# Performance work log

Hardware: AMD Instinct MI355X
Metric: run time of the kernel (lower is better)

The kernel has to match this reference:

```python
import jax, jax.numpy as jnp
import numpy as np

EPS = 1e-5

def _bn(x, gamma, beta, mean, var):
    # channel axis = 1; inference-style batchnorm with given stats
    shape = (1, -1) + (1,) * (x.ndim - 2)
    inv = gamma / jnp.sqrt(var + EPS)
    return x * inv.reshape(shape) + (beta - mean * inv).reshape(shape)

def _gather(f, idx):
    # f: (C, N), idx: (N, ns) -> (C, N, ns)
    return f[:, idx]

def setup_inputs() -> dict:
    key = jax.random.key(0)
    ks = jax.random.split(key, 24)
    B, N, C, NS, O = 4, 32768, 64, 16, 128
    inp = {}
    inp['xyz'] = jax.random.normal(ks[0], (B, N, 3), jnp.float32)
    inp['feature'] = jax.random.normal(ks[1], (B, C, N), jnp.float32)
    inp['idx'] = jax.random.randint(ks[2], (B, N, NS), 0, N, jnp.int64 if jax.config.jax_enable_x64 else jnp.int32)
    inp['W1'] = jax.random.normal(ks[3], (64, 3), jnp.float32)
    inp['b1'] = jax.random.normal(ks[4], (64,), jnp.float32)
    inp['g1'] = jax.random.uniform(ks[5], (64,), jnp.float32)
    inp['be1'] = jax.random.normal(ks[6], (64,), jnp.float32)
    inp['m1'] = jnp.zeros((64,), jnp.float32)
    inp['v1'] = jnp.ones((64,), jnp.float32)
    inp['W2'] = jax.random.normal(ks[7], (64, 64), jnp.float32)
    inp['b2'] = jax.random.normal(ks[8], (64,), jnp.float32)
    inp['g2'] = jax.random.uniform(ks[9], (64,), jnp.float32)
    inp['be2'] = jax.random.normal(ks[10], (64,), jnp.float32)
    inp['m2'] = jnp.zeros((64,), jnp.float32)
    inp['v2'] = jnp.ones((64,), jnp.float32)
    inp['W3'] = jax.random.normal(ks[11], (64, 64), jnp.float32)
    inp['b3'] = jax.random.normal(ks[12], (64,), jnp.float32)
    inp['Wf'] = jax.random.normal(ks[13], (O, C * 64), jnp.float32)
    inp['bf'] = jax.random.normal(ks[14], (O,), jnp.float32)
    inp['gf'] = jax.random.uniform(ks[15], (O,), jnp.float32)
    inp['bef'] = jax.random.normal(ks[16], (O,), jnp.float32)
    inp['mf'] = jnp.zeros((O,), jnp.float32)
    inp['vf'] = jnp.ones((O,), jnp.float32)
    return inp

def reference(xyz, feature, idx, W1, b1, g1, be1, m1, v1, W2, b2, g2, be2, m2, v2, W3, b3, Wf, bf, gf, bef, mf, vf):
    B, C, N = feature.shape
    xyz_t = jnp.transpose(xyz, (0, 2, 1))  # (B, 3, N)
    # grouped relative positions: (B, 3, N, ns)
    grouped_xyz = jax.vmap(_gather)(xyz_t, idx) - xyz_t[:, :, :, None]
    # WeightNet: Conv2d 1x1 layers on channel dim
    h = jnp.einsum('oc,bcns->bons', W1, grouped_xyz) + b1[None, :, None, None]
    h = jax.nn.relu(_bn(h, g1, be1, m1, v1))
    h = jnp.einsum('oc,bcns->bons', W2, h) + b2[None, :, None, None]
    h = jax.nn.relu(_bn(h, g2, be2, m2, v2))
    weights = jnp.einsum('oc,bcns->bons', W3, h) + b3[None, :, None, None]  # (B, 64, N, ns)
    # gather features per neighbor: (B, C, N, ns)
    gfeat = jax.vmap(_gather)(feature, idx)
    # per-point matmul (B,N,C,ns) @ (B,N,ns,64) -> (B,N,C,64) -> (B,N,C*64)
    agg = jnp.einsum('bcns,bwns->bncw', gfeat, weights).reshape(B, N, C * weights.shape[1])
    # final Conv1d 1x1 + BN + ReLU, output (B, O, N)
    y = jnp.einsum('of,bnf->bon', Wf, agg) + bf[None, :, None]
    return jax.nn.relu(_bn(y, gf, bef, mf, vf))
```

## Files before the change

### kernel.cpp

```cpp
#include <hip/hip_runtime.h>
#include <cstdint>
#include <cstddef>

#define EPSV 1e-5f
constexpr int Bn  = 4;
constexpr int Nn  = 32768;
constexpr int Cn  = 64;
constexpr int NSn = 16;
constexpr int On  = 128;
constexpr int Pn  = 32;
constexpr int MAIN_BLOCKS = Bn * (Nn / Pn);

typedef __attribute__((ext_vector_type(8))) short short8;
typedef __attribute__((ext_vector_type(4))) float f32x4;

static __device__ __forceinline__ unsigned short f2bf(float f) {
  union { float f; unsigned u; } v; v.f = f;
  unsigned r = v.u + 0x7fffu + ((v.u >> 16) & 1u);
  return (unsigned short)(r >> 16);
}
static __device__ __forceinline__ unsigned pack2(unsigned short a, unsigned short b) {
  return (unsigned)a | ((unsigned)b << 16);
}

constexpr size_t WS_FEATT = 0;
constexpr size_t WS_WFP   = 16u * 1024 * 1024;
constexpr size_t WS_PF    = 17u * 1024 * 1024;
constexpr size_t WS_W2F   = WS_PF + 4096;
constexpr size_t WS_W3B   = WS_W2F + 8192;
constexpr size_t WS_WG    = 18u * 1024 * 1024;
constexpr size_t WS_NEED_SPLIT = WS_WG + (size_t)Bn * Nn * 1024 * 2;

__global__ void k_params(const float* __restrict__ W1, const float* __restrict__ b1,
                         const float* __restrict__ g1, const float* __restrict__ be1,
                         const float* __restrict__ m1, const float* __restrict__ v1,
                         const float* __restrict__ W2, const float* __restrict__ b2,
                         const float* __restrict__ g2, const float* __restrict__ be2,
                         const float* __restrict__ m2, const float* __restrict__ v2,
                         const float* __restrict__ W3, const float* __restrict__ b3,
                         const float* __restrict__ bf_, const float* __restrict__ gf,
                         const float* __restrict__ bef, const float* __restrict__ mf,
                         const float* __restrict__ vf,
                         float* __restrict__ pf, unsigned short* __restrict__ W2f,
                         unsigned short* __restrict__ W3b) {
  int t = threadIdx.x;
  if (t < 64) {
    float inv1 = g1[t] * rsqrtf(v1[t] + EPSV);
    pf[t * 4 + 0] = W1[t * 3 + 0] * inv1;
    pf[t * 4 + 1] = W1[t * 3 + 1] * inv1;
    pf[t * 4 + 2] = W1[t * 3 + 2] * inv1;
    pf[t * 4 + 3] = 0.f;
    pf[256 + t] = b1[t] * inv1 + be1[t] - m1[t] * inv1;
    float inv2 = g2[t] * rsqrtf(v2[t] + EPSV);
    pf[320 + t] = b2[t] * inv2 + be2[t] - m2[t] * inv2;
    pf[384 + t] = b3[t];
    for (int k = 0; k < 64; ++k) {
      W2f[t * 64 + k] = f2bf(W2[t * 64 + k] * inv2);
      W3b[t * 64 + k] = f2bf(W3[t * 64 + k]);
    }
  }
  if (t < 128) {
    float invf = gf[t] * rsqrtf(vf[t] + EPSV);
    pf[448 + t] = bf_[t] * invf + bef[t] - mf[t] * invf;
  }
}

__global__ void k_featT(const float* __restrict__ feat, unsigned short* __restrict__ featT) {
  int blk = blockIdx.x;
  int b = blk >> 9;
  int n0 = (blk & 511) << 6;
  __shared__ float tile[64][65];
  int t = threadIdx.x;
  int n_in = t & 63;
  int c4 = t >> 6;
  const float* fb = feat + (size_t)b * Cn * Nn;
#pragma unroll
  for (int k = 0; k < 16; ++k) {
    int c = c4 * 16 + k;
    tile[c][n_in] = fb[(size_t)c * Nn + n0 + n_in];
  }
  __syncthreads();
  unsigned short* outp = featT + ((size_t)b * Nn + n0) * Cn;
  int cc = t & 63;
#pragma unroll
  for (int k = 0; k < 16; ++k) {
    int nn = c4 * 16 + k;
    outp[(size_t)nn * Cn + cc] = f2bf(tile[cc][nn]);
  }
}

__global__ void k_wfp(const float* __restrict__ Wf, const float* __restrict__ gf,
                      const float* __restrict__ vf, unsigned short* __restrict__ WfP) {
  int e = blockIdx.x * 256 + threadIdx.x;
  int rec = e >> 9, wi_ = e & 511;
  int l = wi_ >> 3, j = wi_ & 7;
  int q = rec >> 6, ks = (rec >> 3) & 7, ot = rec & 7;
  int o = ot * 16 + (l & 15);
  int kk = ks * 32 + (l >> 4) * 8 + j;
  int c = (q >> 2) * 16 + (kk >> 4);
  int w = (q & 3) * 16 + (kk & 15);
  float invf = gf[o] * rsqrtf(vf[o] + EPSV);
  WfP[e] = f2bf(Wf[(size_t)o * 4096 + c * 64 + w] * invf);
}

constexpr int SMEM_WNET = 73728;

__launch_bounds__(512, 4)
__global__ void k_wnet(const float* __restrict__ xyz, const int* __restrict__ idx,
                       const float* __restrict__ pf,
                       const unsigned short* __restrict__ W2f,
                       const unsigned short* __restrict__ W3b,
                       unsigned short* __restrict__ wg) {
  extern __shared__ __align__(16) char smem[];
  unsigned short* h1 = (unsigned short*)(smem);
  unsigned short* h2 = (unsigned short*)(smem + 32768);
  float4* gxbuf = (float4*)(smem + 65536);

  const int t = threadIdx.x;
  const int lane = t & 63;
  const int wv = t >> 6;
  const int lq = lane >> 4;
  const int lm = lane & 15;
  const int blk = blockIdx.x;
  const int bb = blk >> 10;
  const int n0 = (blk & 1023) * Pn;

  const float* W1f = pf;
  const float* b1f = pf + 256;
  const float* b2f = pf + 320;
  const float* b3f = pf + 384;
  const f32x4 z4 = {0.f, 0.f, 0.f, 0.f};

  if (t < 256) {
    const float* xb = xyz + (size_t)bb * Nn * 3;
#pragma unroll
    for (int a = 0; a < 2; ++a) {
      int col = t + a * 256;
      int p_ = col >> 4, s_ = col & 15;
      int iv = idx[((size_t)bb * Nn + n0 + p_) * NSn + s_];
      float cx = xb[(size_t)(n0 + p_) * 3 + 0];
      float cy = xb[(size_t)(n0 + p_) * 3 + 1];
      float cz = xb[(size_t)(n0 + p_) * 3 + 2];
      gxbuf[col] = make_float4(xb[(size_t)iv * 3 + 0] - cx,
                               xb[(size_t)iv * 3 + 1] - cy,
                               xb[(size_t)iv * 3 + 2] - cz, 0.f);
    }
  }
  __syncthreads();

  for (int h = 0; h < 2; ++h) {
    if (wv < 4) {
#pragma unroll
      for (int a = 0; a < 8; ++a) {
        int aid = t + a * 256;
        int col = aid & 255;
        int oct = aid >> 8;
        float4 g = gxbuf[h * 256 + col];
        unsigned short vals[8];
#pragma unroll
        for (int jj = 0; jj < 8; ++jj) {
          int ch = oct * 8 + jj;
          float v = W1f[ch * 4 + 0] * g.x + W1f[ch * 4 + 1] * g.y +
                    W1f[ch * 4 + 2] * g.z + b1f[ch];
          vals[jj] = f2bf(fmaxf(v, 0.f));
        }
        int u = oct ^ (col & 7);
        uint4 wv4;
        wv4.x = pack2(vals[0], vals[1]); wv4.y = pack2(vals[2], vals[3]);
        wv4.z = pack2(vals[4], vals[5]); wv4.w = pack2(vals[6], vals[7]);
        *(uint4*)(h1 + (size_t)col * 64 + u * 8) = wv4;
      }
    }
    __syncthreads();

    if (wv < 4) {
      f32x4 acc2[4][4];
#pragma unroll
      for (int mt = 0; mt < 4; ++mt)
#pragma unroll
        for (int nt = 0; nt < 4; ++nt) acc2[mt][nt] = z4;
      short8 afr[4][2];
#pragma unroll
      for (int mt = 0; mt < 4; ++mt)
#pragma unroll
        for (int ks = 0; ks < 2; ++ks)
          afr[mt][ks] = *(const short8*)(W2f + (mt * 16 + lm) * 64 + ks * 32 + lq * 8);
#pragma unroll
      for (int nt = 0; nt < 4; ++nt) {
        int col = wv * 64 + nt * 16 + lm;
#pragma unroll
        for (int ks = 0; ks < 2; ++ks) {
          int u = (ks * 4 + lq) ^ (col & 7);
          short8 bfr = *(short8*)(h1 + (size_t)col * 64 + u * 8);
#pragma unroll
          for (int mt = 0; mt < 4; ++mt)
            acc2[mt][nt] = __builtin_amdgcn_mfma_f32_16x16x32_bf16(afr[mt][ks], bfr, acc2[mt][nt], 0, 0, 0);
        }
      }
#pragma unroll
      for (int mt = 0; mt < 4; ++mt)
#pragma unroll
        for (int nt = 0; nt < 4; ++nt) {
          int col = wv * 64 + nt * 16 + lm;
#pragma unroll
          for (int r = 0; r < 4; ++r) {
            int ch = mt * 16 + lq * 4 + r;
            float v = fmaxf(acc2[mt][nt][r] + b2f[ch], 0.f);
            int u = (ch >> 3) ^ (col & 7);
            h2[(size_t)col * 64 + u * 8 + (ch & 7)] = f2bf(v);
          }
        }
    }
    __syncthreads();

    if (wv < 4) {
      f32x4 acc3[4][4];
#pragma unroll
      for (int mt = 0; mt < 4; ++mt)
#pragma unroll
        for (int nt = 0; nt < 4; ++nt) acc3[mt][nt] = z4;
      short8 afr[4][2];
#pragma unroll
      for (int mt = 0; mt < 4; ++mt)
#pragma unroll
        for (int ks = 0; ks < 2; ++ks)
          afr[mt][ks] = *(const short8*)(W3b + (mt * 16 + lm) * 64 + ks * 32 + lq * 8);
#pragma unroll
      for (int nt = 0; nt < 4; ++nt) {
        int col = wv * 64 + nt * 16 + lm;
#pragma unroll
        for (int ks = 0; ks < 2; ++ks) {
          int u = (ks * 4 + lq) ^ (col & 7);
          short8 bfr = *(short8*)(h2 + (size_t)col * 64 + u * 8);
#pragma unroll
          for (int mt = 0; mt < 4; ++mt)
            acc3[mt][nt] = __builtin_amdgcn_mfma_f32_16x16x32_bf16(afr[mt][ks], bfr, acc3[mt][nt], 0, 0, 0);
        }
      }
#pragma unroll
      for (int nt = 0; nt < 4; ++nt) {
        int pl = wv * 4 + nt;
        int p_ = h * 16 + pl;
        int s_ = lm;
        size_t pg = (size_t)((size_t)bb * Nn + n0 + p_) * 1024;
#pragma unroll
        for (int mt = 0; mt < 4; ++mt)
#pragma unroll
          for (int r = 0; r < 4; ++r) {
            int w_ = mt * 16 + lq * 4 + r;
            float v = acc3[mt][nt][r] + b3f[w_];
            wg[pg + (s_ >> 3) * 512 + w_ * 8 + (s_ & 7)] = f2bf(v);
          }
      }
    }
    __syncthreads();
  }
}

constexpr int SMEM_FINAL = 49664;

__launch_bounds__(512, 4)
__global__ void k_final(const int* __restrict__ idx,
                        const unsigned short* __restrict__ featT,
                        const unsigned short* __restrict__ WfP,
                        const float* __restrict__ pf,
                        const unsigned short* __restrict__ wg,
                        float* __restrict__ outp) {
  extern __shared__ __align__(16) char smem[];
  unsigned short* gbuf   = (unsigned short*)(smem);
  unsigned short* aggbuf = (unsigned short*)(smem + 16896);

  const int t = threadIdx.x;
  const int lane = t & 63;
  const int wv = t >> 6;
  const int lq = lane >> 4;
  const int lm = lane & 15;
  const int blk = blockIdx.x;
  const int bb = blk >> 10;
  const int n0 = (blk & 1023) * Pn;

  const short8 z8 = {0, 0, 0, 0, 0, 0, 0, 0};
  const f32x4  z4 = {0.f, 0.f, 0.f, 0.f};

  const int p0 = t >> 4, s0 = t & 15;
  const int iv = idx[((size_t)bb * Nn + n0 + p0) * NSn + s0];
  const unsigned short* fsrc = featT + ((size_t)bb * Nn + iv) * 64;
  const unsigned short* afbase = wg + ((size_t)((size_t)bb * Nn + n0 + wv * 4) * 1024)
                                    + (lq & 1) * 512 + lm * 8;

  f32x4 accY[2] = {z4, z4};

  for (int ci = 0; ci < 4; ++ci) {
    {
      uint4 d0 = *(const uint4*)(fsrc + ci * 16);
      uint4 d1 = *(const uint4*)(fsrc + ci * 16 + 8);
      unsigned uu[8] = {d0.x, d0.y, d0.z, d0.w, d1.x, d1.y, d1.z, d1.w};
      size_t base = (size_t)p0 * 264 + (s0 >> 3) * 128 + (s0 & 7);
#pragma unroll
      for (int k = 0; k < 8; ++k) {
        gbuf[base + (2 * k) * 8]     = (unsigned short)(uu[k] & 0xffffu);
        gbuf[base + (2 * k + 1) * 8] = (unsigned short)(uu[k] >> 16);
      }
    }
    __syncthreads();

    short8 bfr[4];
#pragma unroll
    for (int pp = 0; pp < 4; ++pp) {
      int p_ = wv * 4 + pp;
      short8 v = *(short8*)(gbuf + (size_t)p_ * 264 + (lq & 1) * 128 + lm * 8);
      bfr[pp] = (lq < 2) ? v : z8;
    }

#pragma unroll
    for (int wi = 0; wi < 4; ++wi) {
      int q = ci * 4 + wi;
      int buf = q & 1;
      short8 wf[8];
#pragma unroll
      for (int ks = 0; ks < 4; ++ks)
        wf[ks] = *(const short8*)(WfP + ((size_t)((q * 8 + ks) * 8 + wv)) * 512 + lane * 8);
#pragma unroll
      for (int pp = 0; pp < 4; ++pp) {
        int p_ = wv * 4 + pp;
        short8 afv = *(const short8*)(afbase + (size_t)pp * 1024 + wi * 128);
        short8 afr = (lq < 2) ? afv : z8;
        f32x4 d = __builtin_amdgcn_mfma_f32_16x16x32_bf16(afr, bfr[pp], z4, 0, 0, 0);
        int kkb = lm * 16 + lq * 4;
        int us = (kkb >> 3) ^ (p_ & 7);
        uint2 w2v;
        w2v.x = pack2(f2bf(d[0]), f2bf(d[1]));
        w2v.y = pack2(f2bf(d[2]), f2bf(d[3]));
        *(uint2*)(aggbuf + (size_t)buf * 8192 + (size_t)p_ * 256 + us * 8 + (kkb & 7)) = w2v;
      }
      __syncthreads();
#pragma unroll
      for (int ks = 4; ks < 8; ++ks)
        wf[ks] = *(const short8*)(WfP + ((size_t)((q * 8 + ks) * 8 + wv)) * 512 + lane * 8);
#pragma unroll
      for (int ks = 0; ks < 8; ++ks) {
#pragma unroll
        for (int mt = 0; mt < 2; ++mt) {
          int p16 = mt * 16 + lm;
          int u = (ks * 4 + lq) ^ (p16 & 7);
          short8 afr = *(const short8*)(aggbuf + (size_t)buf * 8192 + (size_t)p16 * 256 + u * 8);
          accY[mt] = __builtin_amdgcn_mfma_f32_16x16x32_bf16(afr, wf[ks], accY[mt], 0, 0, 0);
        }
      }
    }
  }

  {
    int o = wv * 16 + lm;
    float bo = pf[448 + o];
#pragma unroll
    for (int mt = 0; mt < 2; ++mt) {
      f32x4 vv;
#pragma unroll
      for (int r = 0; r < 4; ++r) vv[r] = fmaxf(accY[mt][r] + bo, 0.f);
      int p_ = mt * 16 + lq * 4;
      float* dst = outp + ((size_t)bb * On + o) * Nn + n0 + p_;
      *(f32x4*)dst = vv;
    }
  }
}

constexpr int SMEM_MAIN = 141312;

__launch_bounds__(512, 1)
__global__ void k_main(const float* __restrict__ xyz, const int* __restrict__ idx,
                       const unsigned short* __restrict__ featT,
                       const unsigned short* __restrict__ WfP,
                       const float* __restrict__ pf,
                       const unsigned short* __restrict__ W2f,
                       const unsigned short* __restrict__ W3b,
                       float* __restrict__ outp) {
  extern __shared__ __align__(16) char smem[];
  unsigned short* wbuf   = (unsigned short*)(smem);
  unsigned short* h1     = (unsigned short*)(smem + 65536);
  unsigned short* gbuf   = (unsigned short*)(smem + 65536);
  unsigned short* h2     = (unsigned short*)(smem + 98304);
  unsigned short* aggbuf = (unsigned short*)(smem + 98304);
  float4* gxbuf = (float4*)(smem + 131072);
  int*    idxbuf = (int*)(smem + 139264);

  const int t = threadIdx.x;
  const int lane = t & 63;
  const int wv = t >> 6;
  const int lq = lane >> 4;
  const int lm = lane & 15;
  const int blk = blockIdx.x;
  const int bb = blk >> 10;
  const int n0 = (blk & 1023) * Pn;

  const float* W1f = pf;
  const float* b1f = pf + 256;
  const float* b2f = pf + 320;
  const float* b3f = pf + 384;
  const float* bff = pf + 448;

  const short8 z8 = {0, 0, 0, 0, 0, 0, 0, 0};
  const f32x4  z4 = {0.f, 0.f, 0.f, 0.f};

  if (t < 256) {
    const float* xb = xyz + (size_t)bb * Nn * 3;
#pragma unroll
    for (int a = 0; a < 2; ++a) {
      int col = t + a * 256;
      int p_ = col >> 4, s_ = col & 15;
      int iv = idx[((size_t)bb * Nn + n0 + p_) * NSn + s_];
      idxbuf[col] = iv;
      float cx = xb[(size_t)(n0 + p_) * 3 + 0];
      float cy = xb[(size_t)(n0 + p_) * 3 + 1];
      float cz = xb[(size_t)(n0 + p_) * 3 + 2];
      gxbuf[col] = make_float4(xb[(size_t)iv * 3 + 0] - cx,
                               xb[(size_t)iv * 3 + 1] - cy,
                               xb[(size_t)iv * 3 + 2] - cz, 0.f);
    }
  }
  __syncthreads();

  for (int h = 0; h < 2; ++h) {
    if (wv < 4) {
#pragma unroll
      for (int a = 0; a < 8; ++a) {
        int aid = t + a * 256;
        int col = aid & 255;
        int oct = aid >> 8;
        float4 g = gxbuf[h * 256 + col];
        unsigned short vals[8];
#pragma unroll
        for (int jj = 0; jj < 8; ++jj) {
          int ch = oct * 8 + jj;
          float v = W1f[ch * 4 + 0] * g.x + W1f[ch * 4 + 1] * g.y +
                    W1f[ch * 4 + 2] * g.z + b1f[ch];
          vals[jj] = f2bf(fmaxf(v, 0.f));
        }
        int u = oct ^ (col & 7);
        uint4 wv4;
        wv4.x = pack2(vals[0], vals[1]); wv4.y = pack2(vals[2], vals[3]);
        wv4.z = pack2(vals[4], vals[5]); wv4.w = pack2(vals[6], vals[7]);
        *(uint4*)(h1 + (size_t)col * 64 + u * 8) = wv4;
      }
    }
    __syncthreads();

    if (wv < 4) {
      f32x4 acc2[4][4];
#pragma unroll
      for (int mt = 0; mt < 4; ++mt)
#pragma unroll
        for (int nt = 0; nt < 4; ++nt) acc2[mt][nt] = z4;
      short8 afr[4][2];
#pragma unroll
      for (int mt = 0; mt < 4; ++mt)
#pragma unroll
        for (int ks = 0; ks < 2; ++ks)
          afr[mt][ks] = *(const short8*)(W2f + (mt * 16 + lm) * 64 + ks * 32 + lq * 8);
#pragma unroll
      for (int nt = 0; nt < 4; ++nt) {
        int col = wv * 64 + nt * 16 + lm;
#pragma unroll
        for (int ks = 0; ks < 2; ++ks) {
          int u = (ks * 4 + lq) ^ (col & 7);
          short8 bfr = *(short8*)(h1 + (size_t)col * 64 + u * 8);
#pragma unroll
          for (int mt = 0; mt < 4; ++mt)
            acc2[mt][nt] = __builtin_amdgcn_mfma_f32_16x16x32_bf16(afr[mt][ks], bfr, acc2[mt][nt], 0, 0, 0);
        }
      }
#pragma unroll
      for (int mt = 0; mt < 4; ++mt)
#pragma unroll
        for (int nt = 0; nt < 4; ++nt) {
          int col = wv * 64 + nt * 16 + lm;
#pragma unroll
          for (int r = 0; r < 4; ++r) {
            int ch = mt * 16 + lq * 4 + r;
            float v = fmaxf(acc2[mt][nt][r] + b2f[ch], 0.f);
            int u = (ch >> 3) ^ (col & 7);
            h2[(size_t)col * 64 + u * 8 + (ch & 7)] = f2bf(v);
          }
        }
    }
    __syncthreads();

    if (wv < 4) {
      f32x4 acc3[4][4];
#pragma unroll
      for (int mt = 0; mt < 4; ++mt)
#pragma unroll
        for (int nt = 0; nt < 4; ++nt) acc3[mt][nt] = z4;
      short8 afr[4][2];
#pragma unroll
      for (int mt = 0; mt < 4; ++mt)
#pragma unroll
        for (int ks = 0; ks < 2; ++ks)
          afr[mt][ks] = *(const short8*)(W3b + (mt * 16 + lm) * 64 + ks * 32 + lq * 8);
#pragma unroll
      for (int nt = 0; nt < 4; ++nt) {
        int col = wv * 64 + nt * 16 + lm;
#pragma unroll
        for (int ks = 0; ks < 2; ++ks) {
          int u = (ks * 4 + lq) ^ (col & 7);
          short8 bfr = *(short8*)(h2 + (size_t)col * 64 + u * 8);
#pragma unroll
          for (int mt = 0; mt < 4; ++mt)
            acc3[mt][nt] = __builtin_amdgcn_mfma_f32_16x16x32_bf16(afr[mt][ks], bfr, acc3[mt][nt], 0, 0, 0);
        }
      }
#pragma unroll
      for (int nt = 0; nt < 4; ++nt) {
        int pl = wv * 4 + nt;
        int p_ = h * 16 + pl;
        int s_ = lm;
#pragma unroll
        for (int mt = 0; mt < 4; ++mt)
#pragma unroll
          for (int r = 0; r < 4; ++r) {
            int w_ = mt * 16 + lq * 4 + r;
            float v = acc3[mt][nt][r] + b3f[w_];
            wbuf[(size_t)p_ * 1024 + (s_ >> 3) * 512 + w_ * 8 + (s_ & 7)] = f2bf(v);
          }
      }
    }
    __syncthreads();
  }

  f32x4 accY[2] = {z4, z4};

  for (int ci = 0; ci < 4; ++ci) {
    {
      int sl = t;
      int p_ = sl >> 4, s_ = sl & 15;
      int iv = idxbuf[sl];
      const unsigned short* src = featT + ((size_t)bb * Nn + iv) * 64 + ci * 16;
      uint4 d0 = *(const uint4*)(src);
      uint4 d1 = *(const uint4*)(src + 8);
      unsigned uu[8] = {d0.x, d0.y, d0.z, d0.w, d1.x, d1.y, d1.z, d1.w};
      size_t base = (size_t)p_ * 256 + (s_ >> 3) * 128 + (s_ & 7);
#pragma unroll
      for (int k = 0; k < 8; ++k) {
        gbuf[base + (2 * k) * 8]     = (unsigned short)(uu[k] & 0xffffu);
        gbuf[base + (2 * k + 1) * 8] = (unsigned short)(uu[k] >> 16);
      }
    }
    __syncthreads();

    for (int wi = 0; wi < 4; ++wi) {
      int q = ci * 4 + wi;
      int buf = q & 1;
#pragma unroll
      for (int pp = 0; pp < 4; ++pp) {
        int p_ = wv * 4 + pp;
        short8 afr = z8, bfr = z8;
        if (lq < 2) {
          afr = *(short8*)(wbuf + (size_t)p_ * 1024 + lq * 512 + (wi * 16 + lm) * 8);
          bfr = *(short8*)(gbuf + (size_t)p_ * 256 + lq * 128 + lm * 8);
        }
        f32x4 d = __builtin_amdgcn_mfma_f32_16x16x32_bf16(afr, bfr, z4, 0, 0, 0);
        int kkb = lm * 16 + lq * 4;
        int us = (kkb >> 3) ^ (p_ & 7);
        uint2 w2v;
        w2v.x = pack2(f2bf(d[0]), f2bf(d[1]));
        w2v.y = pack2(f2bf(d[2]), f2bf(d[3]));
        *(uint2*)(aggbuf + (size_t)buf * 8192 + (size_t)p_ * 256 + us * 8 + (kkb & 7)) = w2v;
      }
      __syncthreads();
#pragma unroll
      for (int ks = 0; ks < 8; ++ks) {
        short8 wfr = *(const short8*)(WfP + ((size_t)((q * 8 + ks) * 8 + wv)) * 512 + lane * 8);
#pragma unroll
        for (int mt = 0; mt < 2; ++mt) {
          int p16 = mt * 16 + lm;
          int u = (ks * 4 + lq) ^ (p16 & 7);
          short8 afr = *(const short8*)(aggbuf + (size_t)buf * 8192 + (size_t)p16 * 256 + u * 8);
          accY[mt] = __builtin_amdgcn_mfma_f32_16x16x32_bf16(afr, wfr, accY[mt], 0, 0, 0);
        }
      }
    }
  }

  {
    int o = wv * 16 + lm;
    float bo = bff[o];
#pragma unroll
    for (int mt = 0; mt < 2; ++mt) {
      f32x4 vv;
#pragma unroll
      for (int r = 0; r < 4; ++r) vv[r] = fmaxf(accY[mt][r] + bo, 0.f);
      int p_ = mt * 16 + lq * 4;
      float* dst = outp + ((size_t)bb * On + o) * Nn + n0 + p_;
      *(f32x4*)dst = vv;
    }
  }
}

extern "C" void kernel_launch(void* const* d_in, const int* in_sizes, int n_in,
                              void* d_out, int out_size, void* d_ws, size_t ws_size,
                              hipStream_t stream) {
  const float* xyz  = (const float*)d_in[0];
  const float* feat = (const float*)d_in[1];
  const int*   idx  = (const int*)d_in[2];
  const float* W1 = (const float*)d_in[3];
  const float* b1 = (const float*)d_in[4];
  const float* g1 = (const float*)d_in[5];
  const float* be1 = (const float*)d_in[6];
  const float* m1 = (const float*)d_in[7];
  const float* v1 = (const float*)d_in[8];
  const float* W2 = (const float*)d_in[9];
  const float* b2 = (const float*)d_in[10];
  const float* g2 = (const float*)d_in[11];
  const float* be2 = (const float*)d_in[12];
  const float* m2 = (const float*)d_in[13];
  const float* v2 = (const float*)d_in[14];
  const float* W3 = (const float*)d_in[15];
  const float* b3 = (const float*)d_in[16];
  const float* Wf = (const float*)d_in[17];
  const float* bf_ = (const float*)d_in[18];
  const float* gf = (const float*)d_in[19];
  const float* bef = (const float*)d_in[20];
  const float* mf = (const float*)d_in[21];
  const float* vf = (const float*)d_in[22];

  char* ws = (char*)d_ws;
  unsigned short* featT = (unsigned short*)(ws + WS_FEATT);
  unsigned short* WfP   = (unsigned short*)(ws + WS_WFP);
  float*          pf    = (float*)(ws + WS_PF);
  unsigned short* W2f   = (unsigned short*)(ws + WS_W2F);
  unsigned short* W3b   = (unsigned short*)(ws + WS_W3B);
  unsigned short* wg    = (unsigned short*)(ws + WS_WG);
  float* outp = (float*)d_out;

  hipLaunchKernelGGL(k_params, dim3(1), dim3(256), 0, stream,
                     W1, b1, g1, be1, m1, v1, W2, b2, g2, be2, m2, v2,
                     W3, b3, bf_, gf, bef, mf, vf, pf, W2f, W3b);
  hipLaunchKernelGGL(k_featT, dim3(Bn * (Nn / 64)), dim3(256), 0, stream, feat, featT);
  hipLaunchKernelGGL(k_wfp, dim3(2048), dim3(256), 0, stream, Wf, gf, vf, WfP);

  if (ws_size >= WS_NEED_SPLIT) {
    hipFuncSetAttribute(reinterpret_cast<const void*>(k_wnet),
                        hipFuncAttributeMaxDynamicSharedMemorySize, SMEM_WNET);
    hipFuncSetAttribute(reinterpret_cast<const void*>(k_final),
                        hipFuncAttributeMaxDynamicSharedMemorySize, SMEM_FINAL);
    hipLaunchKernelGGL(k_wnet, dim3(MAIN_BLOCKS), dim3(512), SMEM_WNET, stream,
                       xyz, idx, pf, W2f, W3b, wg);
    hipLaunchKernelGGL(k_final, dim3(MAIN_BLOCKS), dim3(512), SMEM_FINAL, stream,
                       idx, featT, WfP, pf, wg, outp);
  } else {
    hipFuncSetAttribute(reinterpret_cast<const void*>(k_main),
                        hipFuncAttributeMaxDynamicSharedMemorySize, SMEM_MAIN);
    hipLaunchKernelGGL(k_main, dim3(MAIN_BLOCKS), dim3(512), SMEM_MAIN, stream,
                       xyz, idx, featT, WfP, pf, W2f, W3b, outp);
  }
}
```

Before: 680.3 us.

## Slice the split wnet/final pipeline to fit the available workspace

```diff
diff --git a/kernel.cpp b/kernel.cpp
--- a/kernel.cpp
+++ b/kernel.cpp
@@ -29,7 +29,7 @@
 constexpr size_t WS_W2F   = WS_PF + 4096;
 constexpr size_t WS_W3B   = WS_W2F + 8192;
 constexpr size_t WS_WG    = 18u * 1024 * 1024;
-constexpr size_t WS_NEED_SPLIT = WS_WG + (size_t)Bn * Nn * 1024 * 2;
+constexpr size_t WG_PER_BLOCK = (size_t)Pn * 1024 * 2;
 
 __global__ void k_params(const float* __restrict__ W1, const float* __restrict__ b1,
                          const float* __restrict__ g1, const float* __restrict__ be1,
@@ -110,7 +110,7 @@
                        const float* __restrict__ pf,
                        const unsigned short* __restrict__ W2f,
                        const unsigned short* __restrict__ W3b,
-                       unsigned short* __restrict__ wg) {
+                       unsigned short* __restrict__ wg, int sliceStart) {
   extern __shared__ __align__(16) char smem[];
   unsigned short* h1 = (unsigned short*)(smem);
   unsigned short* h2 = (unsigned short*)(smem + 32768);
@@ -121,9 +121,10 @@
   const int wv = t >> 6;
   const int lq = lane >> 4;
   const int lm = lane & 15;
-  const int blk = blockIdx.x;
-  const int bb = blk >> 10;
-  const int n0 = (blk & 1023) * Pn;
+  const int blkFlat = sliceStart + blockIdx.x;
+  const int bb = blkFlat >> 10;
+  const int n0 = (blkFlat & 1023) * Pn;
+  const size_t wgBase = (size_t)blockIdx.x * Pn * 1024;
 
   const float* W1f = pf;
   const float* b1f = pf + 256;
@@ -242,7 +243,7 @@
         int pl = wv * 4 + nt;
         int p_ = h * 16 + pl;
         int s_ = lm;
-        size_t pg = (size_t)((size_t)bb * Nn + n0 + p_) * 1024;
+        size_t pg = wgBase + (size_t)p_ * 1024;
 #pragma unroll
         for (int mt = 0; mt < 4; ++mt)
 #pragma unroll
@@ -265,7 +266,7 @@
                         const unsigned short* __restrict__ WfP,
                         const float* __restrict__ pf,
                         const unsigned short* __restrict__ wg,
-                        float* __restrict__ outp) {
+                        float* __restrict__ outp, int sliceStart) {
   extern __shared__ __align__(16) char smem[];
   unsigned short* gbuf   = (unsigned short*)(smem);
   unsigned short* aggbuf = (unsigned short*)(smem + 16896);
@@ -275,9 +276,9 @@
   const int wv = t >> 6;
   const int lq = lane >> 4;
   const int lm = lane & 15;
-  const int blk = blockIdx.x;
-  const int bb = blk >> 10;
-  const int n0 = (blk & 1023) * Pn;
+  const int blkFlat = sliceStart + blockIdx.x;
+  const int bb = blkFlat >> 10;
+  const int n0 = (blkFlat & 1023) * Pn;
 
   const short8 z8 = {0, 0, 0, 0, 0, 0, 0, 0};
   const f32x4  z4 = {0.f, 0.f, 0.f, 0.f};
@@ -285,7 +286,7 @@
   const int p0 = t >> 4, s0 = t & 15;
   const int iv = idx[((size_t)bb * Nn + n0 + p0) * NSn + s0];
   const unsigned short* fsrc = featT + ((size_t)bb * Nn + iv) * 64;
-  const unsigned short* afbase = wg + ((size_t)((size_t)bb * Nn + n0 + wv * 4) * 1024)
+  const unsigned short* afbase = wg + ((size_t)blockIdx.x * Pn + wv * 4) * 1024
                                     + (lq & 1) * 512 + lm * 8;
 
   f32x4 accY[2] = {z4, z4};
@@ -638,15 +639,25 @@
   hipLaunchKernelGGL(k_featT, dim3(Bn * (Nn / 64)), dim3(256), 0, stream, feat, featT);
   hipLaunchKernelGGL(k_wfp, dim3(2048), dim3(256), 0, stream, Wf, gf, vf, WfP);
 
-  if (ws_size >= WS_NEED_SPLIT) {
+  long long avail = (long long)ws_size - (long long)WS_WG;
+  int sliceBlocks = (avail > 0) ? (int)(avail / (long long)WG_PER_BLOCK) : 0;
+  if (sliceBlocks > MAIN_BLOCKS) sliceBlocks = MAIN_BLOCKS;
+
+  if (sliceBlocks >= 128) {
+    int nslices = (MAIN_BLOCKS + sliceBlocks - 1) / sliceBlocks;
+    sliceBlocks = (MAIN_BLOCKS + nslices - 1) / nslices;
     hipFuncSetAttribute(reinterpret_cast<const void*>(k_wnet),
                         hipFuncAttributeMaxDynamicSharedMemorySize, SMEM_WNET);
     hipFuncSetAttribute(reinterpret_cast<const void*>(k_final),
                         hipFuncAttributeMaxDynamicSharedMemorySize, SMEM_FINAL);
-    hipLaunchKernelGGL(k_wnet, dim3(MAIN_BLOCKS), dim3(512), SMEM_WNET, stream,
-                       xyz, idx, pf, W2f, W3b, wg);
-    hipLaunchKernelGGL(k_final, dim3(MAIN_BLOCKS), dim3(512), SMEM_FINAL, stream,
-                       idx, featT, WfP, pf, wg, outp);
+    for (int s = 0; s < MAIN_BLOCKS; s += sliceBlocks) {
+      int nb = MAIN_BLOCKS - s;
+      if (nb > sliceBlocks) nb = sliceBlocks;
+      hipLaunchKernelGGL(k_wnet, dim3(nb), dim3(512), SMEM_WNET, stream,
+                         xyz, idx, pf, W2f, W3b, wg, s);
+      hipLaunchKernelGGL(k_final, dim3(nb), dim3(512), SMEM_FINAL, stream,
+                         idx, featT, WfP, pf, wg, outp, s);
+    }
   } else {
     hipFuncSetAttribute(reinterpret_cast<const void*>(k_main),
                         hipFuncAttributeMaxDynamicSharedMemorySize, SMEM_MAIN);
```

Result: slower. 720.2 us (+5.9%).
